# Kernel optimization log

Hardware: AMD Instinct MI355X
Metric: run time of the kernel (lower is better)

Reference implementation:

```python
import jax, jax.numpy as jnp
import numpy as np

S, Q, N, T, G = 20000, 32, 200000, 30, 64
D_IN, H, D_SV, D_LANG, D_FUSE = 300, 256, 64, 64, 128

def setup_inputs() -> dict:
    key = jax.random.key(0)
    ks = jax.random.split(key, 20)
    sc = 0.05
    inp = {
        'lang_feat': jax.random.normal(ks[0], (Q, T, D_IN), jnp.float32),
        'supvox_feat': jax.random.normal(ks[1], (S, D_SV), jnp.float32),
        'supvox_coords': jax.random.uniform(ks[2], (S, 3), jnp.float32),
        'lang_len': jax.random.randint(ks[3], (Q,), 5, T + 1).astype(jnp.int32),
        'grps': jax.random.randint(ks[4], (S,), 0, G).astype(jnp.int32),
        'supervox': jax.random.randint(ks[5], (N,), 0, S).astype(jnp.int32),
        'gt': jax.random.randint(ks[6], (N, Q), 0, 2).astype(jnp.int32),
        # GRU params (torch layout: [3H, in])
        'gru_w_ih': sc * jax.random.normal(ks[7], (3 * H, D_IN), jnp.float32),
        'gru_w_hh': sc * jax.random.normal(ks[8], (3 * H, H), jnp.float32),
        'gru_b_ih': sc * jax.random.normal(ks[9], (3 * H,), jnp.float32),
        'gru_b_hh': sc * jax.random.normal(ks[10], (3 * H,), jnp.float32),
        # lang_sqz: Linear(256,64) ReLU Linear(64,64)
        'sqz_w1': sc * jax.random.normal(ks[11], (D_LANG, H), jnp.float32),
        'sqz_b1': sc * jax.random.normal(ks[12], (D_LANG,), jnp.float32),
        'sqz_w2': sc * jax.random.normal(ks[13], (D_LANG, D_LANG), jnp.float32),
        'sqz_b2': sc * jax.random.normal(ks[14], (D_LANG,), jnp.float32),
        # feat_fuse: Linear(131,128) ReLU
        'fuse_w': sc * jax.random.normal(ks[15], (D_FUSE, D_SV + 3 + D_LANG), jnp.float32),
        'fuse_b': sc * jax.random.normal(ks[16], (D_FUSE,), jnp.float32),
        # heat_map: Linear(128,2) (Dropout = identity in eval)
        'heat_w': sc * jax.random.normal(ks[17], (2, D_FUSE), jnp.float32),
        'heat_b': sc * jax.random.normal(ks[18], (2,), jnp.float32),
    }
    return inp

def _gru_last(x, lens, w_ih, w_hh, b_ih, b_hh):
    # x: [Q, T, D_IN]; returns hidden at step lens[q]-1 (pack_padded_sequence semantics)
    def step(h, xt_t):
        xt, t = xt_t  # xt: [Q, D_IN]
        gi = xt @ w_ih.T + b_ih          # [Q, 3H]
        gh = h @ w_hh.T + b_hh           # [Q, 3H]
        ir, iz, inn = jnp.split(gi, 3, -1)
        hr, hz, hn = jnp.split(gh, 3, -1)
        r = jax.nn.sigmoid(ir + hr)
        z = jax.nn.sigmoid(iz + hz)
        n = jnp.tanh(inn + r * hn)
        h_new = (1.0 - z) * n + z * h
        h = jnp.where((t < lens)[:, None], h_new, h)
        return h, None
    h0 = jnp.zeros((x.shape[0], w_hh.shape[1]), x.dtype)
    hT, _ = jax.lax.scan(step, h0, (jnp.swapaxes(x, 0, 1), jnp.arange(x.shape[1])))
    return hT  # [Q, H]

def reference(lang_feat, supvox_feat, supvox_coords, lang_len, grps, supervox, gt,
              gru_w_ih, gru_w_hh, gru_b_ih, gru_b_hh,
              sqz_w1, sqz_b1, sqz_w2, sqz_b2, fuse_w, fuse_b, heat_w, heat_b):
    # language branch
    h = _gru_last(lang_feat, lang_len, gru_w_ih, gru_w_hh, gru_b_ih, gru_b_hh)  # [Q,H]
    lang = jax.nn.relu(h @ sqz_w1.T + sqz_b1) @ sqz_w2.T + sqz_b2               # [Q,64]
    # supervoxel branch: cat(feat, coords) -> [S,67]
    sv = jnp.concatenate([supvox_feat, supvox_coords], -1)
    # feat_fuse on cat(sv, lang): split the weight to avoid materializing [S,Q,131]
    d_sv = sv.shape[-1]
    sv_proj = sv @ fuse_w[:, :d_sv].T           # [S,128]
    lang_proj = lang @ fuse_w[:, d_sv:].T       # [Q,128]
    fused = jax.nn.relu(sv_proj[:, None, :] + lang_proj[None, :, :] + fuse_b)  # [S,Q,128]
    logits = fused @ heat_w.T + heat_b          # [S,Q,2]
    obj_score = jax.nn.softmax(logits, -1)[..., 1]  # [S,Q]
    # cluster-grouped mean score (grps_ one-hot; assumes unique(grps)==arange(G))
    grp_oh = (grps[:, None] == jnp.arange(G)).astype(obj_score.dtype)  # [S,G]
    grp_sum = jnp.einsum('sq,sg->qg', obj_score, grp_oh)               # [Q,G]
    sen_grp_score = grp_sum / grp_oh.sum(0)[None, :]                   # [Q,G]
    best = jnp.argmax(sen_grp_score, -1)        # [Q]
    supvox_sen = grp_oh[:, best]                # [S,Q] binary
    obj_pts = supvox_sen[supervox].astype(jnp.int32)  # [N,Q]
    inter = (obj_pts * gt).sum(0).astype(jnp.float32)
    union = jnp.bitwise_or(obj_pts, gt).sum(0).astype(jnp.float32)
    ious = inter / (union + 1e-5)               # [Q]
    return obj_pts, ious
```

## Files before the change

kernel.cpp:

```cpp
#include <hip/hip_runtime.h>
#include <hip/hip_bf16.h>
#include <math.h>

#define S_TOT 20000
#define Q_TOT 32
#define N_TOT 200000
#define T_MAX 30
#define G_TOT 64
#define D_IN 300
#define H_DIM 256
#define D_SV 64
#define D_LANG 64
#define D_FUSE 128
#define D_CAT 67
#define FW_LD 131
#define SCHUNK 32
#define NBLK3 (S_TOT / SCHUNK)
#define SENT64 0xFFFFFFFFFFFFFFFFull
#define PCHUNK 16
#define PTILES 40

#define GI_MT 32
#define GI_NT 64
#define GI_KC 100
#define GI_NB 12
#define GI_GRID (30 * GI_NB)
#define HG_ELEMS (30 * Q_TOT * H_DIM)

#define SYNCS_N 1024

__device__ __forceinline__ float sigmoidf_(float x) { return 1.0f / (1.0f + expf(-x)); }
__device__ __forceinline__ unsigned long long pack2(float a, float b) {
    return ((unsigned long long)__float_as_uint(b) << 32) | (unsigned long long)__float_as_uint(a);
}

__global__ __launch_bounds__(128) void k_gi(const float* __restrict__ lang_feat,
                                            const float* __restrict__ w_ih,
                                            const float* __restrict__ b_ih,
                                            const float* __restrict__ fuse_w,
                                            const float* __restrict__ sqz_w1,
                                            const float* __restrict__ sqz_w2,
                                            const float* __restrict__ heat_w,
                                            float* __restrict__ gi,
                                            float* __restrict__ fwt,
                                            float* __restrict__ w1t,
                                            float* __restrict__ w2t,
                                            float* __restrict__ wdr,
                                            float* __restrict__ hg,
                                            int* __restrict__ syncs) {
    const int tid = threadIdx.x;
    if (blockIdx.x >= GI_GRID) {
        const int xb = blockIdx.x - GI_GRID;
        if (xb == 0) {
            for (int i = tid; i < FW_LD * D_FUSE; i += 128)
                fwt[(i % FW_LD) * D_FUSE + (i / FW_LD)] = fuse_w[i];
            for (int i = tid; i < D_LANG * H_DIM; i += 128)
                w1t[(i & 255) * D_LANG + (i >> 8)] = sqz_w1[i];
            for (int i = tid; i < D_LANG * D_LANG; i += 128)
                w2t[(i & 63) * D_LANG + (i >> 6)] = sqz_w2[i];
            if (tid < D_FUSE) wdr[tid] = heat_w[D_FUSE + tid] - heat_w[tid];
        } else {
            const int fb = xb - 1;
            const int per4 = HG_ELEMS / 4 / 8;
            float4* dst = (float4*)hg + fb * per4;
            const float4 sv = make_float4(__uint_as_float(0xFFFFFFFFu), __uint_as_float(0xFFFFFFFFu),
                                          __uint_as_float(0xFFFFFFFFu), __uint_as_float(0xFFFFFFFFu));
            for (int i = tid; i < per4; i += 128) dst[i] = sv;
            if (fb == 0) for (int i = tid; i < SYNCS_N; i += 128) syncs[i] = 0;
        }
        return;
    }
    __shared__ float x_l[GI_KC][GI_MT + 1];
    __shared__ float w_l[GI_KC][GI_NT + 1];
    const int mb = blockIdx.x / GI_NB, nb = blockIdx.x % GI_NB;
    const int m0 = mb * GI_MT, n0 = nb * GI_NT;
    const int tq4 = (tid >> 4) * 4, jq4 = (tid & 15) * 4;

    float acc[4][4];
    #pragma unroll
    for (int i = 0; i < 4; ++i)
        #pragma unroll
        for (int j = 0; j < 4; ++j) acc[i][j] = 0.f;

    for (int kc = 0; kc < 3; ++kc) {
        const int k0 = kc * GI_KC;
        for (int i = tid; i < GI_MT * GI_KC; i += 128) {
            const int r = i / GI_KC, k = i % GI_KC;
            const int row = m0 + r, q = row / T_MAX, t = row - q * T_MAX;
            x_l[k][r] = lang_feat[(q * T_MAX + t) * D_IN + k0 + k];
        }
        for (int i = tid; i < GI_NT * GI_KC; i += 128) {
            const int r = i / GI_KC, k = i % GI_KC;
            w_l[k][r] = w_ih[(n0 + r) * D_IN + k0 + k];
        }
        __syncthreads();
        #pragma unroll 2
        for (int k = 0; k < GI_KC; ++k) {
            const float x0 = x_l[k][tq4 + 0], x1 = x_l[k][tq4 + 1];
            const float x2 = x_l[k][tq4 + 2], x3 = x_l[k][tq4 + 3];
            const float v0 = w_l[k][jq4 + 0], v1 = w_l[k][jq4 + 1];
            const float v2 = w_l[k][jq4 + 2], v3 = w_l[k][jq4 + 3];
            acc[0][0] = fmaf(x0, v0, acc[0][0]); acc[0][1] = fmaf(x0, v1, acc[0][1]);
            acc[0][2] = fmaf(x0, v2, acc[0][2]); acc[0][3] = fmaf(x0, v3, acc[0][3]);
            acc[1][0] = fmaf(x1, v0, acc[1][0]); acc[1][1] = fmaf(x1, v1, acc[1][1]);
            acc[1][2] = fmaf(x1, v2, acc[1][2]); acc[1][3] = fmaf(x1, v3, acc[1][3]);
            acc[2][0] = fmaf(x2, v0, acc[2][0]); acc[2][1] = fmaf(x2, v1, acc[2][1]);
            acc[2][2] = fmaf(x2, v2, acc[2][2]); acc[2][3] = fmaf(x2, v3, acc[2][3]);
            acc[3][0] = fmaf(x3, v0, acc[3][0]); acc[3][1] = fmaf(x3, v1, acc[3][1]);
            acc[3][2] = fmaf(x3, v2, acc[3][2]); acc[3][3] = fmaf(x3, v3, acc[3][3]);
        }
        __syncthreads();
    }
    const float b0 = b_ih[n0 + jq4 + 0], b1 = b_ih[n0 + jq4 + 1];
    const float b2 = b_ih[n0 + jq4 + 2], b3 = b_ih[n0 + jq4 + 3];
    #pragma unroll
    for (int i = 0; i < 4; ++i) {
        const int row = m0 + tq4 + i;
        const int q = row / T_MAX, t = row - q * T_MAX;
        float4 v = make_float4(acc[i][0] + b0, acc[i][1] + b1, acc[i][2] + b2, acc[i][3] + b3);
        *(float4*)&gi[(q * T_MAX + t) * 768 + n0 + jq4] = v;
    }
}

__global__ __launch_bounds__(384, 1) void k_gru8(const float* __restrict__ gi,
                                                 const float* __restrict__ w_hh,
                                                 const float* __restrict__ b_hh,
                                                 const int* __restrict__ lang_len,
                                                 float* __restrict__ hg,
                                                 float* __restrict__ hbuf,
                                                 const float* __restrict__ w1t,
                                                 const float* __restrict__ b1,
                                                 const float* __restrict__ w2t,
                                                 const float* __restrict__ b2,
                                                 const float* __restrict__ fwt,
                                                 const float* __restrict__ fuse_b,
                                                 float* __restrict__ langc,
                                                 int* __restrict__ qdone) {
    __shared__ __align__(16) float wlds[96 * 256];
    __shared__ __align__(16) float hlq[4 * 68];
    __shared__ float ghl[96];
    __shared__ float gil[T_MAX * 96];

    const int tid = threadIdx.x;
    const int q = blockIdx.x >> 3, b = blockIdx.x & 7;
    int len = lang_len[q]; if (len > T_MAX) len = T_MAX; if (len < 1) len = 1;

    {
        const float4* src4 = (const float4*)w_hh;
        float4* dst4 = (float4*)wlds;
        for (int i = tid; i < 96 * 64; i += 384) {
            const int r = i >> 6, c = i & 63;
            const int grow = ((r >> 5) << 8) + (b << 5) + (r & 31);
            dst4[r * 64 + (c ^ (r & 7))] = src4[grow * 64 + c];
        }
    }
    for (int i = tid; i < len * 96; i += 384) {
        const int t = i / 96, r = i % 96;
        gil[i] = gi[(q * T_MAX + t) * 768 + ((r >> 5) << 8) + (b << 5) + (r & 31)];
    }
    __syncthreads();

    float hfin = 0.f;
    {
        float hnew = 0.f;
        if (tid < 32) {
            const float bhr = b_hh[(b << 5) + tid];
            const float bhz = b_hh[H_DIM + (b << 5) + tid];
            const float bhn = b_hh[2 * H_DIM + (b << 5) + tid];
            const float r = sigmoidf_(gil[tid] + bhr);
            const float z = sigmoidf_(gil[32 + tid] + bhz);
            const float n = tanhf(gil[64 + tid] + r * bhn);
            hnew = (1.f - z) * n;
            if (len == 1) hfin = hnew;
        }
        if (tid < 64 && len > 1) {
            const float a0 = __shfl(hnew, 2 * (tid & 15));
            const float a1 = __shfl(hnew, 2 * (tid & 15) + 1);
            if (tid < 16) {
                unsigned long long* dst = (unsigned long long*)(hg + q * H_DIM + (b << 5));
                __hip_atomic_store(dst + tid, pack2(a0, a1), __ATOMIC_RELAXED, __HIP_MEMORY_SCOPE_AGENT);
            }
        }
    }

    const int row = tid >> 2, ql = tid & 3;
    const float bh = b_hh[((row >> 5) << 8) + (b << 5) + (row & 31)];
    const int rx = row & 7;
    const float4* wrow4 = (const float4*)wlds + row * 64;
    const int cbase = ql << 4;

    for (int t = 1; t < len; ++t) {
        if (tid < 128) {
            const unsigned long long* src =
                (const unsigned long long*)(hg + (size_t)(t - 1) * (Q_TOT * H_DIM) + q * H_DIM);
            unsigned long long v;
            while ((v = __hip_atomic_load(src + tid, __ATOMIC_RELAXED,
                                          __HIP_MEMORY_SCOPE_AGENT)) == SENT64)
                __builtin_amdgcn_s_sleep(1);
            const int k = 2 * tid;
            const int o = (k >> 6) * 68 + (k & 63);
            hlq[o]     = __uint_as_float((unsigned)(v & 0xffffffffu));
            hlq[o + 1] = __uint_as_float((unsigned)(v >> 32));
        }
        __syncthreads();
        float hold = 0.f;
        if (tid < 32) { const int k = (b << 5) + tid; hold = hlq[(k >> 6) * 68 + (k & 63)]; }
        const float4* h4 = (const float4*)(hlq + ql * 68);
        float ax = 0.f, ay = 0.f, az = 0.f, aw = 0.f;
        #pragma unroll
        for (int i = 0; i < 16; ++i) {
            const float4 wv = wrow4[(cbase + i) ^ rx];
            const float4 hv = h4[i];
            ax = fmaf(wv.x, hv.x, ax);
            ay = fmaf(wv.y, hv.y, ay);
            az = fmaf(wv.z, hv.z, az);
            aw = fmaf(wv.w, hv.w, aw);
        }
        float s = (ax + ay) + (az + aw);
        s += __shfl_xor(s, 1);
        s += __shfl_xor(s, 2);
        if (ql == 0) ghl[row] = s + bh;
        __syncthreads();
        float hnew = 0.f;
        if (tid < 32) {
            const float* gt_ = gil + t * 96;
            const float r = sigmoidf_(gt_[tid] + ghl[tid]);
            const float z = sigmoidf_(gt_[32 + tid] + ghl[32 + tid]);
            const float n = tanhf(gt_[64 + tid] + r * ghl[64 + tid]);
            hnew = (1.f - z) * n + z * hold;
            if (t == len - 1) hfin = hnew;
        }
        if (tid < 64 && t < len - 1) {
            const float a0 = __shfl(hnew, 2 * (tid & 15));
            const float a1 = __shfl(hnew, 2 * (tid & 15) + 1);
            if (tid < 16) {
                unsigned long long* dst =
                    (unsigned long long*)(hg + (size_t)t * (Q_TOT * H_DIM) + q * H_DIM + (b << 5));
                __hip_atomic_store(dst + tid, pack2(a0, a1), __ATOMIC_RELAXED, __HIP_MEMORY_SCOPE_AGENT);
            }
        }
    }

    if (tid < 32)
        __hip_atomic_store(&hbuf[q * H_DIM + (b << 5) + tid], hfin,
                           __ATOMIC_RELAXED, __HIP_MEMORY_SCOPE_AGENT);
    asm volatile("s_waitcnt vmcnt(0)" ::: "memory");
    __syncthreads();
    if (tid == 0)
        __hip_atomic_fetch_add(&qdone[q], 1, __ATOMIC_RELAXED, __HIP_MEMORY_SCOPE_AGENT);
    if (b != 0) return;

    if (tid == 0) {
        while (__hip_atomic_load(&qdone[q], __ATOMIC_RELAXED, __HIP_MEMORY_SCOPE_AGENT) < 8)
            __builtin_amdgcn_s_sleep(2);
    }
    __syncthreads();
    float* hql = gil;
    float* t1l = gil + 256;
    float* lgl = gil + 320;
    if (tid < H_DIM)
        hql[tid] = __hip_atomic_load(&hbuf[q * H_DIM + tid], __ATOMIC_RELAXED, __HIP_MEMORY_SCOPE_AGENT);
    __syncthreads();
    if (tid < 256) {
        const int c = tid >> 2, qq = tid & 3;
        float a = 0.f;
        #pragma unroll 8
        for (int j = 0; j < 64; ++j) {
            const int k = (qq << 6) + j;
            a = fmaf(w1t[k * D_LANG + c], hql[k], a);
        }
        a += __shfl_xor(a, 1);
        a += __shfl_xor(a, 2);
        if (qq == 0) t1l[c] = fmaxf(a + b1[c], 0.f);
    }
    __syncthreads();
    if (tid < 256) {
        const int c = tid >> 2, qq = tid & 3;
        float a = 0.f;
        #pragma unroll
        for (int j = 0; j < 16; ++j) {
            const int k = (qq << 4) + j;
            a = fmaf(w2t[k * D_LANG + c], t1l[k], a);
        }
        a += __shfl_xor(a, 1);
        a += __shfl_xor(a, 2);
        if (qq == 0) lgl[c] = a + b2[c];
    }
    __syncthreads();
    if (tid < 256) {
        const int d = tid >> 1, hh = tid & 1;
        float a = 0.f;
        #pragma unroll 8
        for (int j = 0; j < 32; ++j) {
            const int k = (hh << 5) + j;
            a = fmaf(fwt[(D_CAT + k) * D_FUSE + d], lgl[k], a);
        }
        a += __shfl_xor(a, 1);
        if (hh == 0) langc[q * D_FUSE + d] = a + fuse_b[d];
    }
}

__global__ __launch_bounds__(256, 3) void k_tail(const float* __restrict__ feat,
                                                 const float* __restrict__ coords,
                                                 const int* __restrict__ grps,
                                                 const float* __restrict__ langc,
                                                 const float* __restrict__ fwt,
                                                 const float* __restrict__ wdr_g,
                                                 const float* __restrict__ heat_b,
                                                 float* __restrict__ grp_part,
                                                 int* __restrict__ cnt_part,
                                                 float* __restrict__ grp2,
                                                 int* __restrict__ cnt2,
                                                 int* __restrict__ best,
                                                 const int* __restrict__ supervox,
                                                 const int* __restrict__ gt,
                                                 float* __restrict__ out,
                                                 int* __restrict__ syncs) {
    int* interG = syncs;
    int* unionG = syncs + 32;
    int* t_out  = syncs + 64;
    int* gtick  = syncs + 65;
    int* qtick  = syncs + 98;
    const int tid = threadIdx.x;
    const int bid = blockIdx.x;

    __shared__ __align__(16) float svin[SCHUNK][68];
    __shared__ __align__(16) float svp[SCHUNK][132];
    __shared__ float score[SCHUNK][Q_TOT];
    __shared__ int grps_l[SCHUNK];
    __shared__ float ps[4][G_TOT];
    __shared__ int   pc[4][G_TOT];
    __shared__ float sc[G_TOT];
    __shared__ int bl[Q_TOT];
    __shared__ int gm[G_TOT];
    __shared__ int bi_s[Q_TOT], bu_s[Q_TOT];
    __shared__ int islast;

    {
        const int s0 = bid * SCHUNK;
        const int dsl = tid & 7, q = tid >> 3;
        float lc[16], wdr[16];
        #pragma unroll
        for (int i = 0; i < 16; ++i) {
            const int d = dsl * 16 + i;
            lc[i]  = langc[q * D_FUSE + d];
            wdr[i] = wdr_g[d];
        }
        const float hbd = heat_b[1] - heat_b[0];

        for (int i = tid; i < SCHUNK * D_SV; i += 256) {
            const int r = i >> 6, c = i & 63;
            svin[r][c] = feat[(s0 + r) * D_SV + c];
        }
        if (tid < SCHUNK * 3) { const int r = tid / 3, c = tid % 3; svin[r][D_SV + c] = coords[(s0 + r) * 3 + c]; }
        if (tid < SCHUNK) grps_l[tid] = grps[s0 + tid];
        __syncthreads();

        {
            const int d = tid & 127, sl0 = tid >> 7;
            float acc[16];
            #pragma unroll
            for (int i = 0; i < 16; ++i) acc[i] = 0.f;
            for (int k4 = 0; k4 < 16; ++k4) {
                const float w0 = fwt[(4 * k4 + 0) * D_FUSE + d];
                const float w1 = fwt[(4 * k4 + 1) * D_FUSE + d];
                const float w2 = fwt[(4 * k4 + 2) * D_FUSE + d];
                const float w3 = fwt[(4 * k4 + 3) * D_FUSE + d];
                #pragma unroll
                for (int i = 0; i < 16; ++i) {
                    const float4 xv = *(const float4*)&svin[sl0 + 2 * i][4 * k4];
                    acc[i] = fmaf(xv.x, w0, fmaf(xv.y, w1, fmaf(xv.z, w2, fmaf(xv.w, w3, acc[i]))));
                }
            }
            for (int k = 64; k < D_CAT; ++k) {
                const float wv = fwt[k * D_FUSE + d];
                #pragma unroll
                for (int i = 0; i < 16; ++i)
                    acc[i] = fmaf(svin[sl0 + 2 * i][k], wv, acc[i]);
            }
            #pragma unroll
            for (int i = 0; i < 16; ++i) svp[sl0 + 2 * i][d] = acc[i];
        }
        __syncthreads();

        for (int sl = 0; sl < SCHUNK; ++sl) {
            const float4* sv4 = (const float4*)(&svp[sl][dsl * 16]);
            float part = 0.f;
            #pragma unroll
            for (int j = 0; j < 4; ++j) {
                const float4 v = sv4[j];
                part = fmaf(fmaxf(v.x + lc[4*j+0], 0.f), wdr[4*j+0], part);
                part = fmaf(fmaxf(v.y + lc[4*j+1], 0.f), wdr[4*j+1], part);
                part = fmaf(fmaxf(v.z + lc[4*j+2], 0.f), wdr[4*j+2], part);
                part = fmaf(fmaxf(v.w + lc[4*j+3], 0.f), wdr[4*j+3], part);
            }
            part += __shfl_xor(part, 1);
            part += __shfl_xor(part, 2);
            part += __shfl_xor(part, 4);
            if (dsl == 0) score[sl][q] = sigmoidf_(part + hbd);
        }
        __syncthreads();

        for (int i = 0; i < 8; ++i) {
            const int cell = tid + 256 * i;
            const int qq = cell >> 6, g = cell & 63;
            float sum = 0.f;
            #pragma unroll
            for (int sl = 0; sl < SCHUNK; ++sl)
                sum += (grps_l[sl] == g) ? score[sl][qq] : 0.f;
            __hip_atomic_store(&grp_part[bid * (Q_TOT * G_TOT) + cell], sum,
                               __ATOMIC_RELAXED, __HIP_MEMORY_SCOPE_AGENT);
            if (cell < G_TOT) {
                int c = 0;
                #pragma unroll
                for (int sl = 0; sl < SCHUNK; ++sl) c += (grps_l[sl] == g);
                __hip_atomic_store(&cnt_part[bid * G_TOT + g], c,
                                   __ATOMIC_RELAXED, __HIP_MEMORY_SCOPE_AGENT);
            }
        }
        asm volatile("s_waitcnt vmcnt(0)" ::: "memory");
        __syncthreads();
        if (tid == 0)
            __hip_atomic_fetch_add(&syncs[160 + 32 * (bid / PTILES)], 1,
                                   __ATOMIC_RELAXED, __HIP_MEMORY_SCOPE_AGENT);
    }

    if (bid < Q_TOT * PCHUNK) {
        const int q = bid & 31, c = bid >> 5;
        const int b0 = c * PTILES;
        int b1 = b0 + PTILES; if (b1 > NBLK3) b1 = NBLK3;
        if (tid == 0) {
            int* tc = &syncs[160 + 32 * c];
            const int tgt = b1 - b0;
            while (__hip_atomic_load(tc, __ATOMIC_RELAXED, __HIP_MEMORY_SCOPE_AGENT) < tgt)
                __builtin_amdgcn_s_sleep(4);
        }
        __syncthreads();
        const int bq = tid >> 6, g = tid & 63;
        float acc = 0.f; int cacc = 0;
        for (int b = b0 + bq; b < b1; b += 4) {
            acc  += grp_part[b * (Q_TOT * G_TOT) + q * G_TOT + g];
            cacc += cnt_part[b * G_TOT + g];
        }
        ps[bq][g] = acc; pc[bq][g] = cacc;
        __syncthreads();
        if (tid < G_TOT) {
            const float s = ((ps[0][tid] + ps[1][tid]) + ps[2][tid]) + ps[3][tid];
            const int  cc = ((pc[0][tid] + pc[1][tid]) + pc[2][tid]) + pc[3][tid];
            __hip_atomic_store(&grp2[(c * Q_TOT + q) * G_TOT + tid], s,
                               __ATOMIC_RELAXED, __HIP_MEMORY_SCOPE_AGENT);
            __hip_atomic_store(&cnt2[(c * Q_TOT + q) * G_TOT + tid], cc,
                               __ATOMIC_RELAXED, __HIP_MEMORY_SCOPE_AGENT);
        }
        __shared__ int myturn;
        asm volatile("s_waitcnt vmcnt(0)" ::: "memory");
        if (tid == 0) {
            const int old = __hip_atomic_fetch_add(&qtick[q], 1, __ATOMIC_RELAXED, __HIP_MEMORY_SCOPE_AGENT);
            myturn = (old == PCHUNK - 1) ? 1 : 0;
        }
        __syncthreads();
        if (myturn) {
            if (tid < G_TOT) {
                float s = 0.f; int cc = 0;
                #pragma unroll
                for (int c2 = 0; c2 < PCHUNK; ++c2) {
                    s  += grp2[(c2 * Q_TOT + q) * G_TOT + tid];
                    cc += cnt2[(c2 * Q_TOT + q) * G_TOT + tid];
                }
                sc[tid] = s / (float)cc;
            }
            __syncthreads();
            if (tid == 0) {
                float bv = sc[0]; int bi = 0;
                for (int g2 = 1; g2 < G_TOT; ++g2) if (sc[g2] > bv) { bv = sc[g2]; bi = g2; }
                __hip_atomic_store(&best[q], bi, __ATOMIC_RELAXED, __HIP_MEMORY_SCOPE_AGENT);
                asm volatile("s_waitcnt vmcnt(0)" ::: "memory");
                const int old = __hip_atomic_fetch_add(gtick, 1, __ATOMIC_RELAXED, __HIP_MEMORY_SCOPE_AGENT);
                if (old == Q_TOT - 1) {
                    #pragma unroll
                    for (int f = 0; f < 8; ++f)
                        __hip_atomic_store(&syncs[672 + 32 * f], 1,
                                           __ATOMIC_RELAXED, __HIP_MEMORY_SCOPE_AGENT);
                }
            }
        }
    }

    if (tid == 0) {
        int* fl = &syncs[672 + 32 * (bid & 7)];
        while (__hip_atomic_load(fl, __ATOMIC_RELAXED, __HIP_MEMORY_SCOPE_AGENT) == 0)
            __builtin_amdgcn_s_sleep(16);
    }
    __syncthreads();

    if (tid < Q_TOT) bl[tid] = best[tid];
    __syncthreads();
    if (tid < G_TOT) {
        int m = 0;
        #pragma unroll
        for (int qq = 0; qq < Q_TOT; ++qq) m |= (bl[qq] == tid) ? (1 << qq) : 0;
        gm[tid] = m;
    }
    __syncthreads();

    {
        const int gidx = bid * 256 + tid;
        const int q4 = (gidx & 7) * 4;
        const int nstride = (NBLK3 * 256) >> 3;
        int a0 = 0, a1 = 0, a2 = 0, a3 = 0;
        int u0 = 0, u1 = 0, u2 = 0, u3 = 0;
        for (int n = gidx >> 3; n < N_TOT; n += nstride) {
            const int m = gm[grps[supervox[n]]];
            const int4 g4 = *(const int4*)&gt[n * Q_TOT + q4];
            const int o0 = (m >> (q4 + 0)) & 1;
            const int o1 = (m >> (q4 + 1)) & 1;
            const int o2 = (m >> (q4 + 2)) & 1;
            const int o3 = (m >> (q4 + 3)) & 1;
            *(float4*)&out[n * Q_TOT + q4] =
                make_float4((float)o0, (float)o1, (float)o2, (float)o3);
            a0 += o0 & g4.x; u0 += o0 | g4.x;
            a1 += o1 & g4.y; u1 += o1 | g4.y;
            a2 += o2 & g4.z; u2 += o2 | g4.z;
            a3 += o3 & g4.w; u3 += o3 | g4.w;
        }
        if (tid < Q_TOT) { bi_s[tid] = 0; bu_s[tid] = 0; }
        __syncthreads();
        atomicAdd(&bi_s[q4 + 0], a0); atomicAdd(&bu_s[q4 + 0], u0);
        atomicAdd(&bi_s[q4 + 1], a1); atomicAdd(&bu_s[q4 + 1], u1);
        atomicAdd(&bi_s[q4 + 2], a2); atomicAdd(&bu_s[q4 + 2], u2);
        atomicAdd(&bi_s[q4 + 3], a3); atomicAdd(&bu_s[q4 + 3], u3);
        __syncthreads();
        if (tid < Q_TOT) { atomicAdd(&interG[tid], bi_s[tid]); atomicAdd(&unionG[tid], bu_s[tid]); }
        asm volatile("s_waitcnt vmcnt(0)" ::: "memory");
        if (tid == 0) {
            const int old = __hip_atomic_fetch_add(t_out, 1, __ATOMIC_RELAXED, __HIP_MEMORY_SCOPE_AGENT);
            islast = (old == NBLK3 - 1) ? 1 : 0;
        }
        __syncthreads();
        if (islast && tid < Q_TOT) {
            const int iv = __hip_atomic_load(&interG[tid], __ATOMIC_RELAXED, __HIP_MEMORY_SCOPE_AGENT);
            const int uv = __hip_atomic_load(&unionG[tid], __ATOMIC_RELAXED, __HIP_MEMORY_SCOPE_AGENT);
            out[(size_t)N_TOT * Q_TOT + tid] = (float)iv / ((float)uv + 1e-5f);
        }
    }
}

extern "C" void kernel_launch(void* const* d_in, const int* in_sizes, int n_in,
                              void* d_out, int out_size, void* d_ws, size_t ws_size,
                              hipStream_t stream) {
    const float* lang_feat = (const float*)d_in[0];
    const float* feat      = (const float*)d_in[1];
    const float* coords    = (const float*)d_in[2];
    const int*   lang_len  = (const int*)d_in[3];
    const int*   grps      = (const int*)d_in[4];
    const int*   supervox  = (const int*)d_in[5];
    const int*   gt        = (const int*)d_in[6];
    const float* w_ih      = (const float*)d_in[7];
    const float* w_hh      = (const float*)d_in[8];
    const float* b_ih      = (const float*)d_in[9];
    const float* b_hh      = (const float*)d_in[10];
    const float* sqz_w1    = (const float*)d_in[11];
    const float* sqz_b1    = (const float*)d_in[12];
    const float* sqz_w2    = (const float*)d_in[13];
    const float* sqz_b2    = (const float*)d_in[14];
    const float* fuse_w    = (const float*)d_in[15];
    const float* fuse_b    = (const float*)d_in[16];
    const float* heat_w    = (const float*)d_in[17];
    const float* heat_b    = (const float*)d_in[18];
    float* out = (float*)d_out;

    float* gi       = (float*)d_ws;
    float* hbuf     = gi + 737280;
    float* langc    = hbuf + 8192;
    float* grp_part = langc + 4096;
    int*   cnt_part = (int*)(grp_part + NBLK3 * 2048);
    int*   best     = cnt_part + NBLK3 * 64;
    int*   syncs    = best + 32;
    float* hg       = (float*)(syncs + SYNCS_N);
    float* fwt      = hg + HG_ELEMS;
    float* w1t      = fwt + FW_LD * D_FUSE;
    float* w2t      = w1t + H_DIM * D_LANG;
    float* wdr      = w2t + D_LANG * D_LANG;
    float* grp2     = wdr + 128;
    int*   cnt2     = (int*)(grp2 + PCHUNK * Q_TOT * G_TOT);

    k_gi   <<<GI_GRID + 9, 128, 0, stream>>>(lang_feat, w_ih, b_ih, fuse_w, sqz_w1, sqz_w2, heat_w,
                                             gi, fwt, w1t, w2t, wdr, hg, syncs);
    k_gru8 <<<Q_TOT * 8, 384, 0, stream>>>(gi, w_hh, b_hh, lang_len, hg, hbuf,
                                           w1t, sqz_b1, w2t, sqz_b2, fwt, fuse_b, langc,
                                           syncs + 66);
    k_tail <<<NBLK3, 256, 0, stream>>>(feat, coords, grps, langc, fwt, wdr, heat_b,
                                       grp_part, cnt_part, grp2, cnt2, best,
                                       supervox, gt, out, syncs);
}
```

Before: 202.7 us.

## Fuse GRU input projection into recurrent kernel and drop gi workspace

Moves the x@W_ih^T input projection out of the standalone k_gi GEMM kernel and into the per-(query, slice) GRU blocks. Each block computes only its 96 gate rows for its query's 30 timesteps, using a shared-memory region that is later reused for the W_hh tile. This removes the global gi round-trip and a kernel's worth of work from the critical path, leaving only a small init kernel. In exchange, each of the 256 GRU blocks redundantly loads its query's lang_feat and does a small GEMM, which lengthens the serial prologue of the recurrent kernel. It also computes all 30 steps regardless of length.

```diff
diff --git a/kernel.cpp b/kernel.cpp
--- a/kernel.cpp
+++ b/kernel.cpp
@@ -19,12 +19,6 @@
 #define SENT64 0xFFFFFFFFFFFFFFFFull
 #define PCHUNK 16
 #define PTILES 40
-
-#define GI_MT 32
-#define GI_NT 64
-#define GI_KC 100
-#define GI_NB 12
-#define GI_GRID (30 * GI_NB)
 #define HG_ELEMS (30 * Q_TOT * H_DIM)
 
 #define SYNCS_N 1024
@@ -34,95 +28,39 @@
     return ((unsigned long long)__float_as_uint(b) << 32) | (unsigned long long)__float_as_uint(a);
 }
 
-__global__ __launch_bounds__(128) void k_gi(const float* __restrict__ lang_feat,
-                                            const float* __restrict__ w_ih,
-                                            const float* __restrict__ b_ih,
-                                            const float* __restrict__ fuse_w,
-                                            const float* __restrict__ sqz_w1,
-                                            const float* __restrict__ sqz_w2,
-                                            const float* __restrict__ heat_w,
-                                            float* __restrict__ gi,
-                                            float* __restrict__ fwt,
-                                            float* __restrict__ w1t,
-                                            float* __restrict__ w2t,
-                                            float* __restrict__ wdr,
-                                            float* __restrict__ hg,
-                                            int* __restrict__ syncs) {
+__global__ __launch_bounds__(128) void k_init(const float* __restrict__ fuse_w,
+                                              const float* __restrict__ sqz_w1,
+                                              const float* __restrict__ sqz_w2,
+                                              const float* __restrict__ heat_w,
+                                              float* __restrict__ fwt,
+                                              float* __restrict__ w1t,
+                                              float* __restrict__ w2t,
+                                              float* __restrict__ wdr,
+                                              float* __restrict__ hg,
+                                              int* __restrict__ syncs) {
     const int tid = threadIdx.x;
-    if (blockIdx.x >= GI_GRID) {
-        const int xb = blockIdx.x - GI_GRID;
-        if (xb == 0) {
-            for (int i = tid; i < FW_LD * D_FUSE; i += 128)
-                fwt[(i % FW_LD) * D_FUSE + (i / FW_LD)] = fuse_w[i];
-            for (int i = tid; i < D_LANG * H_DIM; i += 128)
-                w1t[(i & 255) * D_LANG + (i >> 8)] = sqz_w1[i];
-            for (int i = tid; i < D_LANG * D_LANG; i += 128)
-                w2t[(i & 63) * D_LANG + (i >> 6)] = sqz_w2[i];
-            if (tid < D_FUSE) wdr[tid] = heat_w[D_FUSE + tid] - heat_w[tid];
-        } else {
-            const int fb = xb - 1;
-            const int per4 = HG_ELEMS / 4 / 8;
-            float4* dst = (float4*)hg + fb * per4;
-            const float4 sv = make_float4(__uint_as_float(0xFFFFFFFFu), __uint_as_float(0xFFFFFFFFu),
-                                          __uint_as_float(0xFFFFFFFFu), __uint_as_float(0xFFFFFFFFu));
-            for (int i = tid; i < per4; i += 128) dst[i] = sv;
-            if (fb == 0) for (int i = tid; i < SYNCS_N; i += 128) syncs[i] = 0;
-        }
-        return;
-    }
-    __shared__ float x_l[GI_KC][GI_MT + 1];
-    __shared__ float w_l[GI_KC][GI_NT + 1];
-    const int mb = blockIdx.x / GI_NB, nb = blockIdx.x % GI_NB;
-    const int m0 = mb * GI_MT, n0 = nb * GI_NT;
-    const int tq4 = (tid >> 4) * 4, jq4 = (tid & 15) * 4;
-
-    float acc[4][4];
-    #pragma unroll
-    for (int i = 0; i < 4; ++i)
-        #pragma unroll
-        for (int j = 0; j < 4; ++j) acc[i][j] = 0.f;
-
-    for (int kc = 0; kc < 3; ++kc) {
-        const int k0 = kc * GI_KC;
-        for (int i = tid; i < GI_MT * GI_KC; i += 128) {
-            const int r = i / GI_KC, k = i % GI_KC;
-            const int row = m0 + r, q = row / T_MAX, t = row - q * T_MAX;
-            x_l[k][r] = lang_feat[(q * T_MAX + t) * D_IN + k0 + k];
-        }
-        for (int i = tid; i < GI_NT * GI_KC; i += 128) {
-            const int r = i / GI_KC, k = i % GI_KC;
-            w_l[k][r] = w_ih[(n0 + r) * D_IN + k0 + k];
-        }
-        __syncthreads();
-        #pragma unroll 2
-        for (int k = 0; k < GI_KC; ++k) {
-            const float x0 = x_l[k][tq4 + 0], x1 = x_l[k][tq4 + 1];
-            const float x2 = x_l[k][tq4 + 2], x3 = x_l[k][tq4 + 3];
-            const float v0 = w_l[k][jq4 + 0], v1 = w_l[k][jq4 + 1];
-            const float v2 = w_l[k][jq4 + 2], v3 = w_l[k][jq4 + 3];
-            acc[0][0] = fmaf(x0, v0, acc[0][0]); acc[0][1] = fmaf(x0, v1, acc[0][1]);
-            acc[0][2] = fmaf(x0, v2, acc[0][2]); acc[0][3] = fmaf(x0, v3, acc[0][3]);
-            acc[1][0] = fmaf(x1, v0, acc[1][0]); acc[1][1] = fmaf(x1, v1, acc[1][1]);
-            acc[1][2] = fmaf(x1, v2, acc[1][2]); acc[1][3] = fmaf(x1, v3, acc[1][3]);
-            acc[2][0] = fmaf(x2, v0, acc[2][0]); acc[2][1] = fmaf(x2, v1, acc[2][1]);
-            acc[2][2] = fmaf(x2, v2, acc[2][2]); acc[2][3] = fmaf(x2, v3, acc[2][3]);
-            acc[3][0] = fmaf(x3, v0, acc[3][0]); acc[3][1] = fmaf(x3, v1, acc[3][1]);
-            acc[3][2] = fmaf(x3, v2, acc[3][2]); acc[3][3] = fmaf(x3, v3, acc[3][3]);
-        }
-        __syncthreads();
-    }
-    const float b0 = b_ih[n0 + jq4 + 0], b1 = b_ih[n0 + jq4 + 1];
-    const float b2 = b_ih[n0 + jq4 + 2], b3 = b_ih[n0 + jq4 + 3];
-    #pragma unroll
-    for (int i = 0; i < 4; ++i) {
-        const int row = m0 + tq4 + i;
-        const int q = row / T_MAX, t = row - q * T_MAX;
-        float4 v = make_float4(acc[i][0] + b0, acc[i][1] + b1, acc[i][2] + b2, acc[i][3] + b3);
-        *(float4*)&gi[(q * T_MAX + t) * 768 + n0 + jq4] = v;
+    if (blockIdx.x == 0) {
+        for (int i = tid; i < FW_LD * D_FUSE; i += 128)
+            fwt[(i % FW_LD) * D_FUSE + (i / FW_LD)] = fuse_w[i];
+        for (int i = tid; i < D_LANG * H_DIM; i += 128)
+            w1t[(i & 255) * D_LANG + (i >> 8)] = sqz_w1[i];
+        for (int i = tid; i < D_LANG * D_LANG; i += 128)
+            w2t[(i & 63) * D_LANG + (i >> 6)] = sqz_w2[i];
+        if (tid < D_FUSE) wdr[tid] = heat_w[D_FUSE + tid] - heat_w[tid];
+    } else {
+        const int fb = blockIdx.x - 1;
+        const int per4 = HG_ELEMS / 4 / 8;
+        float4* dst = (float4*)hg + fb * per4;
+        const float4 sv = make_float4(__uint_as_float(0xFFFFFFFFu), __uint_as_float(0xFFFFFFFFu),
+                                      __uint_as_float(0xFFFFFFFFu), __uint_as_float(0xFFFFFFFFu));
+        for (int i = tid; i < per4; i += 128) dst[i] = sv;
+        if (fb == 0) for (int i = tid; i < SYNCS_N; i += 128) syncs[i] = 0;
     }
 }
 
-__global__ __launch_bounds__(384, 1) void k_gru8(const float* __restrict__ gi,
+__global__ __launch_bounds__(384, 1) void k_gru8(const float* __restrict__ lang_feat,
+                                                 const float* __restrict__ w_ih,
+                                                 const float* __restrict__ b_ih,
                                                  const float* __restrict__ w_hh,
                                                  const float* __restrict__ b_hh,
                                                  const int* __restrict__ lang_len,
@@ -136,15 +74,59 @@
                                                  const float* __restrict__ fuse_b,
                                                  float* __restrict__ langc,
                                                  int* __restrict__ qdone) {
-    __shared__ __align__(16) float wlds[96 * 256];
-    __shared__ __align__(16) float hlq[4 * 68];
-    __shared__ float ghl[96];
-    __shared__ float gil[T_MAX * 96];
+    __shared__ __align__(16) unsigned char SM[111360];
+    float* wlds = (float*)SM;
+    float* XL   = (float*)SM;
+    float* WcL  = (float*)(SM + 12480);
+    float* hlq  = (float*)(SM + 98304);
+    float* ghl  = (float*)(SM + 99392);
+    float* gil  = (float*)(SM + 99776);
 
     const int tid = threadIdx.x;
     const int q = blockIdx.x >> 3, b = blockIdx.x & 7;
     int len = lang_len[q]; if (len > T_MAX) len = T_MAX; if (len < 1) len = 1;
 
+    {
+        const int r96 = tid >> 2, tg = tid & 3;
+        const int growI = ((r96 >> 5) << 8) + (b << 5) + (r96 & 31);
+        float gacc[8];
+        #pragma unroll
+        for (int j = 0; j < 8; ++j) gacc[j] = 0.f;
+        for (int kc = 0; kc < 3; ++kc) {
+            const int k0 = kc * 100;
+            for (int i = tid; i < 3000; i += 384) {
+                const int t = i / 100, k = i - 100 * t;
+                XL[t * 104 + k] = lang_feat[(q * T_MAX + t) * D_IN + k0 + k];
+            }
+            for (int i = tid; i < 9600; i += 384) {
+                const int rr = i / 100, k = i - 100 * rr;
+                WcL[rr * 104 + k] =
+                    w_ih[(size_t)(((rr >> 5) << 8) + (b << 5) + (rr & 31)) * D_IN + k0 + k];
+            }
+            __syncthreads();
+            for (int k4 = 0; k4 < 25; ++k4) {
+                const float4 wv = *(const float4*)&WcL[r96 * 104 + 4 * k4];
+                #pragma unroll
+                for (int j = 0; j < 8; ++j) {
+                    const int t = tg + 4 * j;
+                    if (t < 30) {
+                        const float4 xv = *(const float4*)&XL[t * 104 + 4 * k4];
+                        gacc[j] = fmaf(wv.x, xv.x, fmaf(wv.y, xv.y,
+                                  fmaf(wv.z, xv.z, fmaf(wv.w, xv.w, gacc[j]))));
+                    }
+                }
+            }
+            __syncthreads();
+        }
+        {
+            const float bih = b_ih[growI];
+            #pragma unroll
+            for (int j = 0; j < 8; ++j) {
+                const int t = tg + 4 * j;
+                if (t < 30) gil[t * 96 + r96] = gacc[j] + bih;
+            }
+        }
+    }
     {
         const float4* src4 = (const float4*)w_hh;
         float4* dst4 = (float4*)wlds;
@@ -153,10 +135,6 @@
             const int grow = ((r >> 5) << 8) + (b << 5) + (r & 31);
             dst4[r * 64 + (c ^ (r & 7))] = src4[grow * 64 + c];
         }
-    }
-    for (int i = tid; i < len * 96; i += 384) {
-        const int t = i / 96, r = i % 96;
-        gil[i] = gi[(q * T_MAX + t) * 768 + ((r >> 5) << 8) + (b << 5) + (r & 31)];
     }
     __syncthreads();
 
@@ -569,8 +547,7 @@
     const float* heat_b    = (const float*)d_in[18];
     float* out = (float*)d_out;
 
-    float* gi       = (float*)d_ws;
-    float* hbuf     = gi + 737280;
+    float* hbuf     = (float*)d_ws;
     float* langc    = hbuf + 8192;
     float* grp_part = langc + 4096;
     int*   cnt_part = (int*)(grp_part + NBLK3 * 2048);
@@ -584,11 +561,11 @@
     float* grp2     = wdr + 128;
     int*   cnt2     = (int*)(grp2 + PCHUNK * Q_TOT * G_TOT);
 
-    k_gi   <<<GI_GRID + 9, 128, 0, stream>>>(lang_feat, w_ih, b_ih, fuse_w, sqz_w1, sqz_w2, heat_w,
-                                             gi, fwt, w1t, w2t, wdr, hg, syncs);
-    k_gru8 <<<Q_TOT * 8, 384, 0, stream>>>(gi, w_hh, b_hh, lang_len, hg, hbuf,
-                                           w1t, sqz_b1, w2t, sqz_b2, fwt, fuse_b, langc,
-                                           syncs + 66);
+    k_init <<<9, 128, 0, stream>>>(fuse_w, sqz_w1, sqz_w2, heat_w,
+                                   fwt, w1t, w2t, wdr, hg, syncs);
+    k_gru8 <<<Q_TOT * 8, 384, 0, stream>>>(lang_feat, w_ih, b_ih, w_hh, b_hh, lang_len,
+                                           hg, hbuf, w1t, sqz_b1, w2t, sqz_b2, fwt, fuse_b,
+                                           langc, syncs + 66);
     k_tail <<<NBLK3, 256, 0, stream>>>(feat, coords, grps, langc, fwt, wdr, heat_b,
                                        grp_part, cnt_part, grp2, cnt2, best,
                                        supervox, gt, out, syncs);
```

New measurement: 233.3 us. 15.1% more time.
